# Kernel optimization log

Measured on AMD Instinct MI355X. Metric: run time of the kernel, lower is better.

The kernel has to match this reference:

```python
import jax, jax.numpy as jnp
import numpy as np
from jax import lax

NUM_CLASSES = 13
H, W = 120, 160
INLIER_THRESHOLD = 0.9
LABEL_THRESHOLD = 500
THRESHOLD_VOTE = 10.0
THRESHOLD_PERCENTAGE = 0.02
SKIP_PIXELS = 16


def setup_inputs() -> dict:
    key = jax.random.key(0)
    k0, k1, k2, k3 = jax.random.split(key, 4)
    labels = jax.random.randint(k0, (1, H, W), 0, NUM_CLASSES, dtype=jnp.int32)
    masks = jnp.ones((1, H, W), jnp.int32)
    vertex_pred = jax.random.normal(k1, (1, 3 * NUM_CLASSES, H, W), jnp.float32)
    extents = jax.random.uniform(k2, (NUM_CLASSES, 3), jnp.float32, 0.05, 0.3)
    poses = jax.random.normal(k3, (1, 13), jnp.float32)
    # flattened 3x3 intrinsics K: fx=meta[0], px=meta[2], fy=meta[4], py=meta[5]
    meta_data = jnp.array([[500.0, 0.0, W / 2.0, 0.0, 500.0, H / 2.0, 0.0, 0.0, 1.0]], jnp.float32)
    return {"labels": labels, "masks": masks, "vertex_pred": vertex_pred,
            "extents": extents, "poses": poses, "meta_data": meta_data}


def _hough_forward(labels, masks, vertex_pred, extents, poses, meta_data):
    B = labels.shape[0]
    HW = H * W
    ys, xs = jnp.meshgrid(jnp.arange(H, dtype=jnp.float32),
                          jnp.arange(W, dtype=jnp.float32), indexing="ij")
    coords_g = jnp.stack([xs.reshape(-1), ys.reshape(-1)], axis=1)  # [HW,2] center candidates
    samp = jnp.arange(0, HW, SKIP_PIXELS)                            # subsampled voting pixels
    coords_p = coords_g[samp]                                        # [P,2]

    def per_image(args):
        lab, msk, vp, meta = args
        lab_f = lab.reshape(-1)
        valid_pix = msk.reshape(-1) > 0
        fx, fy, pxc, pyc = meta[0], meta[4], meta[2], meta[5]

        def per_class(c):
            mask_full = (lab_f == c) & valid_pix            # [HW]
            num_label = jnp.sum(mask_full)
            labeled_p = mask_full[samp]                     # [P]
            vpc = lax.dynamic_slice_in_dim(vp, 3 * c, 3, axis=0)  # [3,H,W]
            dx = vpc[0].reshape(-1)[samp]
            dy = vpc[1].reshape(-1)[samp]
            dz_full = vpc[2].reshape(-1)
            dn = jnp.sqrt(dx * dx + dy * dy) + 1e-6
            dxn, dyn = dx / dn, dy / dn
            # displacement from each voting pixel to every candidate center: [P,HW]
            ddx = coords_g[None, :, 0] - coords_p[:, None, 0]
            ddy = coords_g[None, :, 1] - coords_p[:, None, 1]
            dist = jnp.sqrt(ddx * ddx + ddy * ddy)
            cosang = (ddx * dxn[:, None] + ddy * dyn[:, None]) / jnp.maximum(dist, 1e-6)
            inlier = (cosang > INLIER_THRESHOLD) & (dist > 0.0) & labeled_p[:, None]
            votes = jnp.sum(inlier.astype(jnp.float32), axis=0)  # [HW] Hough accumulator
            best = jnp.argmax(votes)
            vmax = votes[best]
            cx, cy = coords_g[best, 0], coords_g[best, 1]
            # depth: exp of mean predicted log-depth over this class's pixels
            msum = jnp.maximum(num_label.astype(jnp.float32), 1.0)
            z = jnp.exp(jnp.sum(dz_full * mask_full.astype(jnp.float32)) / msum)
            z = jnp.maximum(z, 1e-3)
            bw = extents[c, 0] * fx / z
            bh = extents[c, 1] * fy / z
            nsamp = jnp.maximum(jnp.sum(labeled_p).astype(jnp.float32), 1.0)
            valid = (vmax >= THRESHOLD_VOTE) & (num_label >= LABEL_THRESHOLD) & \
                    (vmax >= THRESHOLD_PERCENTAGE * nsamp)
            cf = c.astype(jnp.float32)
            box = jnp.stack([cf, cx - bw / 2, cy - bh / 2, cx + bw / 2, cy + bh / 2, vmax])
            tx = (cx - pxc) * z / fx
            ty = (cy - pyc) * z / fy
            one = jnp.ones_like(z)
            zero = jnp.zeros_like(z)
            pose = jnp.stack([one, zero, zero, zero, tx, ty, z])  # identity quat + translation
            onehot = (jnp.arange(4 * NUM_CLASSES) // 4 == c).astype(jnp.float32)
            weight = valid.astype(jnp.float32) * onehot
            target = jnp.zeros((4 * NUM_CLASSES,), jnp.float32)
            return box, pose, target, weight

        return lax.map(per_class, jnp.arange(1, NUM_CLASSES))

    boxes, poses_o, targets, weights = lax.map(per_image, (labels, masks, vertex_pred, meta_data))
    Cm1 = NUM_CLASSES - 1
    N = B * Cm1
    bidx = jnp.repeat(jnp.arange(B, dtype=jnp.float32), Cm1)[:, None]
    top_box = jnp.concatenate([bidx, boxes.reshape(N, 6)], axis=1)      # [N,7]
    top_pose = poses_o.reshape(N, 7)
    top_target = targets.reshape(N, 4 * NUM_CLASSES)
    top_weight = weights.reshape(N, 4 * NUM_CLASSES)
    top_domain = jnp.repeat(jnp.arange(B, dtype=jnp.int32), Cm1)
    return top_box, top_pose, top_target, top_weight, top_domain


def reference(labels, masks, vertex_pred, extents, poses, meta_data):
    return _hough_forward(labels, masks, vertex_pred, extents, poses, meta_data)
```

## Files before the change

### kernel.cpp

```cpp
#include <hip/hip_runtime.h>
#include <hip/hip_bf16.h>

#define NCLS 13
#define HH 120
#define WW 160
#define HWSZ (HH * WW)
#define PSAMP 1200
#define CM1 (NCLS - 1)
#define NBLK 75
#define NVOTE (NBLK * CM1)

#define C_HI 0.8100011f
#define C_LO 0.8099988f


__global__ void hough_prep(const int* __restrict__ labels,
                           const int* __restrict__ masks,
                           const float* __restrict__ vp,
                           float4* __restrict__ praw,
                           int* __restrict__ bcnt,
                           int* __restrict__ pcnt,
                           float* __restrict__ pdz,
                           int* __restrict__ best13) {
    const int tid = threadIdx.x;
    const int b = blockIdx.x;
    const int i = b * 256 + tid;
    __shared__ int lcnt[CM1];
    if (tid < CM1) lcnt[tid] = 0;
    if (b == 0 && tid < CM1 + 1) best13[tid] = 0;
    __syncthreads();

    const int lab = labels[i];
    const bool valid = (lab > 0) && (masks[i] > 0);
    const int cls = valid ? lab - 1 : -1;
    float dz = 0.f;
    if (valid) dz = vp[(3 * lab + 2) * HWSZ + i];

    if (valid && ((tid & 15) == 0)) {
        float dx = vp[(3 * lab + 0) * HWSZ + i];
        float dy = vp[(3 * lab + 1) * HWSZ + i];
        float dn = __fadd_rn(
            __fsqrt_rn(__fadd_rn(__fmul_rn(dx, dx), __fmul_rn(dy, dy))), 1e-6f);
        int k = atomicAdd(&lcnt[cls], 1);
        praw[(cls * NBLK + b) * 16 + k] =
            make_float4((float)(i % WW), (float)(i / WW),
                        __fdiv_rn(dx, dn), __fdiv_rn(dy, dn));
    }

    __shared__ float s_dz[4][CM1];
    __shared__ int   s_ct[4][CM1];
    const int w = tid >> 6, lane = tid & 63;
    for (int c1 = 0; c1 < CM1; ++c1) {
        unsigned long long bl = __ballot(cls == c1);
        float v = (cls == c1) ? dz : 0.f;
        for (int off = 32; off > 0; off >>= 1) v += __shfl_xor(v, off);
        if (lane == 0) { s_ct[w][c1] = (int)__popcll(bl); s_dz[w][c1] = v; }
    }
    __syncthreads();
    if (tid < CM1) {
        bcnt[tid * NBLK + b] = lcnt[tid];
        pcnt[tid * NBLK + b] = s_ct[0][tid] + s_ct[1][tid] + s_ct[2][tid] + s_ct[3][tid];
        pdz [tid * NBLK + b] = ((s_dz[0][tid] + s_dz[1][tid]) + s_dz[2][tid]) + s_dz[3][tid];
    }
}

__global__ void hough_vote_out(const float4* __restrict__ praw,
                               const int* __restrict__ bcnt,
                               const int* __restrict__ pcnt,
                               const float* __restrict__ pdz,
                               const float* __restrict__ extents,
                               const float* __restrict__ meta,
                               int* __restrict__ best13,
                               float* __restrict__ out) {
    const int c1 = blockIdx.y;
    const int g  = blockIdx.x * 256 + threadIdx.x;
    const int tid = threadIdx.x;
    __shared__ float4 s[PSAMP];
    __shared__ int scnt[NBLK];
    __shared__ int s_n;
    __shared__ int wmax[4];
    __shared__ int is_last;
    if (tid == 0) s_n = 0;
    if (tid < NBLK) scnt[tid] = bcnt[c1 * NBLK + tid];
    __syncthreads();
    for (int t = tid; t < NBLK * 16; t += 256) {
        const int b2 = t >> 4, k = t & 15;
        if (k < scnt[b2]) {
            int pos = atomicAdd(&s_n, 1);
            s[pos] = praw[(c1 * NBLK + b2) * 16 + k];
        }
    }
    __syncthreads();
    const int n = s_n;

    const float xg = (float)(g % WW);
    const float yg = (float)(g / WW);
    int v = 0;
    for (int j = 0; j < n; ++j) {
        float4 e = s[j];
        float ddx = __fsub_rn(xg, e.x);
        float ddy = __fsub_rn(yg, e.y);
        float d2  = __fadd_rn(__fmul_rn(ddx, ddx), __fmul_rn(ddy, ddy));
        float t2  = __fadd_rn(__fmul_rn(ddx, e.z), __fmul_rn(ddy, e.w));
        float q  = t2 * t2;
        float hi = C_HI * d2;
        float lo = C_LO * d2;
        bool in;
        if (q <= hi && q >= lo) {
            float dist = __fsqrt_rn(d2);
            float cosang = __fdiv_rn(t2, fmaxf(dist, 1e-6f));
            in = (cosang > 0.9f) && (dist > 0.0f);
        } else {
            in = (t2 > 0.0f) && (q > hi);
        }
        v += in ? 1 : 0;
    }

    int key = (v << 15) | (19199 - g);
    for (int off = 32; off > 0; off >>= 1) {
        int o = __shfl_xor(key, off);
        key = key > o ? key : o;
    }
    if ((tid & 63) == 0) wmax[tid >> 6] = key;
    __syncthreads();
    if (tid == 0) {
        int k01 = wmax[0] > wmax[1] ? wmax[0] : wmax[1];
        int k23 = wmax[2] > wmax[3] ? wmax[2] : wmax[3];
        atomicMax(&best13[c1], k01 > k23 ? k01 : k23);
        __threadfence();
        int old = atomicAdd(&best13[CM1], 1);
        is_last = (old == NVOTE - 1) ? 1 : 0;
    }
    __syncthreads();
    if (!is_last) return;

    __threadfence();
    float* top_box    = out;
    float* top_pose   = out + 84;
    float* top_target = out + 168;
    float* top_weight = out + 792;
    float* top_domain = out + 1416;

    for (int j = tid; j < 624; j += 256) top_target[j] = 0.f;
    if (tid >= 244) top_domain[tid - 244] = 0.f;

    __shared__ int   r_nl[CM1][16];
    __shared__ int   r_ns[CM1][16];
    __shared__ float r_dz[CM1][16];
    if (tid < CM1 * 16) {
        const int cc = tid >> 4, l = tid & 15;
        int nl = 0, ns = 0; float ds = 0.f;
        for (int b = l; b < NBLK; b += 16) {
            nl += pcnt[cc * NBLK + b];
            ns += bcnt[cc * NBLK + b];
            ds += pdz [cc * NBLK + b];
        }
        r_nl[cc][l] = nl; r_ns[cc][l] = ns; r_dz[cc][l] = ds;
    }
    __syncthreads();
    for (int st = 8; st > 0; st >>= 1) {
        if (tid < CM1 * 16) {
            const int cc = tid >> 4, l = tid & 15;
            if (l < st) {
                r_nl[cc][l] += r_nl[cc][l + st];
                r_ns[cc][l] += r_ns[cc][l + st];
                r_dz[cc][l] += r_dz[cc][l + st];
            }
        }
        __syncthreads();
    }

    if (tid < CM1) {
        const int cc = tid, c = tid + 1;
        const int nl = r_nl[cc][0];
        const int ns = r_ns[cc][0];
        const float ds = r_dz[cc][0];
        const int key2 = atomicMax(&best13[cc], 0);
        const float vmax = (float)(key2 >> 15);
        const int bi = 19199 - (key2 & 32767);
        const float cx = (float)(bi % WW);
        const float cy = (float)(bi / WW);
        const float msum = fmaxf((float)nl, 1.0f);
        float z = expf(ds / msum);
        z = fmaxf(z, 1e-3f);
        const float fx = meta[0], fy = meta[4], pxc = meta[2], pyc = meta[5];
        const float bw = extents[c * 3 + 0] * fx / z;
        const float bh = extents[c * 3 + 1] * fy / z;
        const float nsamp = fmaxf((float)ns, 1.0f);
        const bool valid = (vmax >= 10.0f) && (nl >= 500) &&
                           (vmax >= 0.02f * nsamp);

        float* bx = top_box + cc * 7;
        bx[0] = 0.0f;
        bx[1] = (float)c;
        bx[2] = cx - bw * 0.5f;
        bx[3] = cy - bh * 0.5f;
        bx[4] = cx + bw * 0.5f;
        bx[5] = cy + bh * 0.5f;
        bx[6] = vmax;

        const float tx = (cx - pxc) * z / fx;
        const float ty = (cy - pyc) * z / fy;
        float* ps = top_pose + cc * 7;
        ps[0] = 1.f; ps[1] = 0.f; ps[2] = 0.f; ps[3] = 0.f;
        ps[4] = tx;  ps[5] = ty;  ps[6] = z;

        float* wt = top_weight + cc * 52;
        const float wv = valid ? 1.0f : 0.0f;
        for (int j = 0; j < 52; ++j)
            wt[j] = ((j >> 2) == c) ? wv : 0.0f;
    }
}

extern "C" void kernel_launch(void* const* d_in, const int* in_sizes, int n_in,
                              void* d_out, int out_size, void* d_ws, size_t ws_size,
                              hipStream_t stream) {
    const int*   labels  = (const int*)d_in[0];
    const int*   masks   = (const int*)d_in[1];
    const float* vp      = (const float*)d_in[2];
    const float* extents = (const float*)d_in[3];
    const float* meta    = (const float*)d_in[5];
    float* out = (float*)d_out;

    char* ws = (char*)d_ws;
    float4* praw   = (float4*)(ws + 0);
    int*    bcnt   = (int*)   (ws + 230400);
    int*    pcnt   = (int*)   (ws + 234000);
    float*  pdz    = (float*) (ws + 237600);
    int*    best13 = (int*)   (ws + 241200);

    hough_prep<<<dim3(NBLK), dim3(256), 0, stream>>>(labels, masks, vp,
                                                     praw, bcnt, pcnt, pdz, best13);
    hough_vote_out<<<dim3(NBLK, CM1), dim3(256), 0, stream>>>(
        praw, bcnt, pcnt, pdz, extents, meta, best13, out);
}
```

Before: 44.30 us.

## Fuse prep and vote kernels into single launch with per-block voter rebuild

Merges the preprocessing and voting kernels into one launch. Each block recomputes its class's subsampled voter list straight from the inputs instead of reading staged buffers. Per-block maxima replace global atomicMax, and the last block reduces them. This removes one kernel launch and the staging round trip, at the cost of redundant voter reconstruction in all 900 blocks. It also relies on a never-reset completion counter taken modulo the block count.

```diff
diff --git a/kernel.cpp b/kernel.cpp
--- a/kernel.cpp
+++ b/kernel.cpp
@@ -14,85 +14,65 @@
 #define C_LO 0.8099988f
 
 
-__global__ void hough_prep(const int* __restrict__ labels,
-                           const int* __restrict__ masks,
-                           const float* __restrict__ vp,
-                           float4* __restrict__ praw,
-                           int* __restrict__ bcnt,
-                           int* __restrict__ pcnt,
-                           float* __restrict__ pdz,
-                           int* __restrict__ best13) {
+__global__ void __launch_bounds__(256) hough_all(
+    const int* __restrict__ labels,
+    const int* __restrict__ masks,
+    const float* __restrict__ vp,
+    const float* __restrict__ extents,
+    const float* __restrict__ meta,
+    int* __restrict__ pcnt,
+    float* __restrict__ pdz,
+    int* __restrict__ bbest,
+    int* __restrict__ bns,
+    unsigned int* __restrict__ done,
+    float* __restrict__ out)
+{
+    const int bid = blockIdx.x;
+    const int c1  = bid / NBLK;
+    const int b   = bid - c1 * NBLK;
+    const int c   = c1 + 1;
     const int tid = threadIdx.x;
-    const int b = blockIdx.x;
-    const int i = b * 256 + tid;
-    __shared__ int lcnt[CM1];
-    if (tid < CM1) lcnt[tid] = 0;
-    if (b == 0 && tid < CM1 + 1) best13[tid] = 0;
-    __syncthreads();
-
-    const int lab = labels[i];
-    const bool valid = (lab > 0) && (masks[i] > 0);
-    const int cls = valid ? lab - 1 : -1;
-    float dz = 0.f;
-    if (valid) dz = vp[(3 * lab + 2) * HWSZ + i];
-
-    if (valid && ((tid & 15) == 0)) {
-        float dx = vp[(3 * lab + 0) * HWSZ + i];
-        float dy = vp[(3 * lab + 1) * HWSZ + i];
-        float dn = __fadd_rn(
-            __fsqrt_rn(__fadd_rn(__fmul_rn(dx, dx), __fmul_rn(dy, dy))), 1e-6f);
-        int k = atomicAdd(&lcnt[cls], 1);
-        praw[(cls * NBLK + b) * 16 + k] =
-            make_float4((float)(i % WW), (float)(i / WW),
-                        __fdiv_rn(dx, dn), __fdiv_rn(dy, dn));
-    }
-
-    __shared__ float s_dz[4][CM1];
-    __shared__ int   s_ct[4][CM1];
-    const int w = tid >> 6, lane = tid & 63;
-    for (int c1 = 0; c1 < CM1; ++c1) {
-        unsigned long long bl = __ballot(cls == c1);
-        float v = (cls == c1) ? dz : 0.f;
-        for (int off = 32; off > 0; off >>= 1) v += __shfl_xor(v, off);
-        if (lane == 0) { s_ct[w][c1] = (int)__popcll(bl); s_dz[w][c1] = v; }
-    }
-    __syncthreads();
-    if (tid < CM1) {
-        bcnt[tid * NBLK + b] = lcnt[tid];
-        pcnt[tid * NBLK + b] = s_ct[0][tid] + s_ct[1][tid] + s_ct[2][tid] + s_ct[3][tid];
-        pdz [tid * NBLK + b] = ((s_dz[0][tid] + s_dz[1][tid]) + s_dz[2][tid]) + s_dz[3][tid];
-    }
-}
-
-__global__ void hough_vote_out(const float4* __restrict__ praw,
-                               const int* __restrict__ bcnt,
-                               const int* __restrict__ pcnt,
-                               const float* __restrict__ pdz,
-                               const float* __restrict__ extents,
-                               const float* __restrict__ meta,
-                               int* __restrict__ best13,
-                               float* __restrict__ out) {
-    const int c1 = blockIdx.y;
-    const int g  = blockIdx.x * 256 + threadIdx.x;
-    const int tid = threadIdx.x;
+
     __shared__ float4 s[PSAMP];
-    __shared__ int scnt[NBLK];
-    __shared__ int s_n;
-    __shared__ int wmax[4];
-    __shared__ int is_last;
+    __shared__ int   s_n;
+    __shared__ float s_dzw[4];
+    __shared__ int   s_ctw[4];
+    __shared__ int   wmax[4];
+    __shared__ int   is_last;
+
     if (tid == 0) s_n = 0;
-    if (tid < NBLK) scnt[tid] = bcnt[c1 * NBLK + tid];
-    __syncthreads();
-    for (int t = tid; t < NBLK * 16; t += 256) {
-        const int b2 = t >> 4, k = t & 15;
-        if (k < scnt[b2]) {
-            int pos = atomicAdd(&s_n, 1);
-            s[pos] = praw[(c1 * NBLK + b2) * 16 + k];
+    __syncthreads();
+
+    {
+        const int i = b * 256 + tid;
+        const int lab = labels[i];
+        const bool m = (lab == c) && (masks[i] > 0);
+        float dzv = m ? vp[(3 * c + 2) * HWSZ + i] : 0.f;
+        unsigned long long bl = __ballot(m);
+        for (int off = 32; off > 0; off >>= 1) dzv += __shfl_xor(dzv, off);
+        if ((tid & 63) == 0) {
+            s_ctw[tid >> 6] = (int)__popcll(bl);
+            s_dzw[tid >> 6] = dzv;
+        }
+    }
+
+    for (int p = tid; p < PSAMP; p += 256) {
+        const int i = p << 4;
+        if (labels[i] == c && masks[i] > 0) {
+            float dx = vp[(3 * c + 0) * HWSZ + i];
+            float dy = vp[(3 * c + 1) * HWSZ + i];
+            float dn = __fadd_rn(
+                __fsqrt_rn(__fadd_rn(__fmul_rn(dx, dx), __fmul_rn(dy, dy))),
+                1e-6f);
+            int k = atomicAdd(&s_n, 1);
+            s[k] = make_float4((float)(i % WW), (float)(i / WW),
+                               __fdiv_rn(dx, dn), __fdiv_rn(dy, dn));
         }
     }
     __syncthreads();
     const int n = s_n;
 
+    const int g = b * 256 + tid;
     const float xg = (float)(g % WW);
     const float yg = (float)(g / WW);
     int v = 0;
@@ -123,18 +103,22 @@
     }
     if ((tid & 63) == 0) wmax[tid >> 6] = key;
     __syncthreads();
+
     if (tid == 0) {
         int k01 = wmax[0] > wmax[1] ? wmax[0] : wmax[1];
         int k23 = wmax[2] > wmax[3] ? wmax[2] : wmax[3];
-        atomicMax(&best13[c1], k01 > k23 ? k01 : k23);
+        bbest[bid] = k01 > k23 ? k01 : k23;
+        pcnt[bid]  = s_ctw[0] + s_ctw[1] + s_ctw[2] + s_ctw[3];
+        pdz[bid]   = ((s_dzw[0] + s_dzw[1]) + s_dzw[2]) + s_dzw[3];
+        bns[c1]    = n;
         __threadfence();
-        int old = atomicAdd(&best13[CM1], 1);
-        is_last = (old == NVOTE - 1) ? 1 : 0;
+        unsigned int old = atomicAdd(done, 1u);
+        is_last = ((old % (unsigned)NVOTE) == (unsigned)(NVOTE - 1)) ? 1 : 0;
     }
     __syncthreads();
     if (!is_last) return;
-
     __threadfence();
+
     float* top_box    = out;
     float* top_pose   = out + 84;
     float* top_target = out + 168;
@@ -145,17 +129,18 @@
     if (tid >= 244) top_domain[tid - 244] = 0.f;
 
     __shared__ int   r_nl[CM1][16];
-    __shared__ int   r_ns[CM1][16];
     __shared__ float r_dz[CM1][16];
+    __shared__ int   r_bk[CM1][16];
     if (tid < CM1 * 16) {
         const int cc = tid >> 4, l = tid & 15;
-        int nl = 0, ns = 0; float ds = 0.f;
-        for (int b = l; b < NBLK; b += 16) {
-            nl += pcnt[cc * NBLK + b];
-            ns += bcnt[cc * NBLK + b];
-            ds += pdz [cc * NBLK + b];
-        }
-        r_nl[cc][l] = nl; r_ns[cc][l] = ns; r_dz[cc][l] = ds;
+        int nl = 0; float ds = 0.f; int bk = 0;
+        for (int bb = l; bb < NBLK; bb += 16) {
+            nl += pcnt[cc * NBLK + bb];
+            ds += pdz [cc * NBLK + bb];
+            int kk = bbest[cc * NBLK + bb];
+            bk = kk > bk ? kk : bk;
+        }
+        r_nl[cc][l] = nl; r_dz[cc][l] = ds; r_bk[cc][l] = bk;
     }
     __syncthreads();
     for (int st = 8; st > 0; st >>= 1) {
@@ -163,19 +148,20 @@
             const int cc = tid >> 4, l = tid & 15;
             if (l < st) {
                 r_nl[cc][l] += r_nl[cc][l + st];
-                r_ns[cc][l] += r_ns[cc][l + st];
                 r_dz[cc][l] += r_dz[cc][l + st];
+                int kk = r_bk[cc][l + st];
+                if (kk > r_bk[cc][l]) r_bk[cc][l] = kk;
             }
         }
         __syncthreads();
     }
 
     if (tid < CM1) {
-        const int cc = tid, c = tid + 1;
+        const int cc = tid, c2 = tid + 1;
         const int nl = r_nl[cc][0];
-        const int ns = r_ns[cc][0];
+        const int ns = bns[cc];
         const float ds = r_dz[cc][0];
-        const int key2 = atomicMax(&best13[cc], 0);
+        const int key2 = r_bk[cc][0];
         const float vmax = (float)(key2 >> 15);
         const int bi = 19199 - (key2 & 32767);
         const float cx = (float)(bi % WW);
@@ -184,15 +170,15 @@
         float z = expf(ds / msum);
         z = fmaxf(z, 1e-3f);
         const float fx = meta[0], fy = meta[4], pxc = meta[2], pyc = meta[5];
-        const float bw = extents[c * 3 + 0] * fx / z;
-        const float bh = extents[c * 3 + 1] * fy / z;
+        const float bw = extents[c2 * 3 + 0] * fx / z;
+        const float bh = extents[c2 * 3 + 1] * fy / z;
         const float nsamp = fmaxf((float)ns, 1.0f);
         const bool valid = (vmax >= 10.0f) && (nl >= 500) &&
                            (vmax >= 0.02f * nsamp);
 
         float* bx = top_box + cc * 7;
         bx[0] = 0.0f;
-        bx[1] = (float)c;
+        bx[1] = (float)c2;
         bx[2] = cx - bw * 0.5f;
         bx[3] = cy - bh * 0.5f;
         bx[4] = cx + bw * 0.5f;
@@ -208,7 +194,7 @@
         float* wt = top_weight + cc * 52;
         const float wv = valid ? 1.0f : 0.0f;
         for (int j = 0; j < 52; ++j)
-            wt[j] = ((j >> 2) == c) ? wv : 0.0f;
+            wt[j] = ((j >> 2) == c2) ? wv : 0.0f;
     }
 }
 
@@ -223,14 +209,12 @@
     float* out = (float*)d_out;
 
     char* ws = (char*)d_ws;
-    float4* praw   = (float4*)(ws + 0);
-    int*    bcnt   = (int*)   (ws + 230400);
-    int*    pcnt   = (int*)   (ws + 234000);
-    float*  pdz    = (float*) (ws + 237600);
-    int*    best13 = (int*)   (ws + 241200);
-
-    hough_prep<<<dim3(NBLK), dim3(256), 0, stream>>>(labels, masks, vp,
-                                                     praw, bcnt, pcnt, pdz, best13);
-    hough_vote_out<<<dim3(NBLK, CM1), dim3(256), 0, stream>>>(
-        praw, bcnt, pcnt, pdz, extents, meta, best13, out);
+    int*          pcnt  = (int*)          (ws + 0);
+    float*        pdz   = (float*)        (ws + 3600);
+    int*          bbest = (int*)          (ws + 7200);
+    int*          bns   = (int*)          (ws + 10800);
+    unsigned int* done  = (unsigned int*) (ws + 10848);
+
+    hough_all<<<dim3(NVOTE), dim3(256), 0, stream>>>(
+        labels, masks, vp, extents, meta, pcnt, pdz, bbest, bns, done, out);
 }
```

New measurement: 61.84 us. 1.4x slower.
